# Kernel optimization log

Measured on AMD Instinct MI355X. Metric: run time of the kernel, lower is better.

## Reference

```python
import jax, jax.numpy as jnp
import numpy as np

DEG = 16

def setup_inputs() -> dict:
    key = jax.random.key(0)
    k1, k2 = jax.random.split(key)
    x = jax.random.uniform(k1, (2097152,), dtype=jnp.float32)  # in [0,1) subset of acos domain
    a = jax.random.normal(k2, (32, DEG), dtype=jnp.float32)
    return {"x": x, "a": a}

def reference(x, a):
    # Chebyshev basis T_k(x) = cos(k * acos(x)), shape [N, deg]
    k = jnp.arange(DEG, dtype=x.dtype)
    basis = jnp.cos(k[None, :] * jnp.arccos(x.reshape(-1))[:, None])  # [N, deg]
    coeffs = a.reshape(-1, DEG)  # [M, deg]
    # out[m, n] = sum_d coeffs[m, d] * basis[n, d]  -- a GEMM, not a 3D broadcast
    return jnp.einsum('md,nd->mn', coeffs, basis)
```

## Files before the change

kernel.cpp:

```cpp
#include <hip/hip_runtime.h>


#define DEG 16
#define M_ROWS 32
#define ELEMS_PER_THREAD 4

typedef __attribute__((ext_vector_type(2))) float f32x2;

__global__ __launch_bounds__(512) void dup_coeff_kernel(
    const float* __restrict__ a, f32x2* __restrict__ ad)
{
    const int i = threadIdx.x;
    if (i < M_ROWS * DEG) {
        const float c = a[i];
        f32x2 v; v.x = c; v.y = c;
        ad[i] = v;
    }
}

__global__ __launch_bounds__(256) void cheb_gemm_kernel(
    const float* __restrict__ x,
    const f32x2* __restrict__ ad,
    float* __restrict__ out,
    int n)
{
    const int i = (blockIdx.x * 256 + threadIdx.x) * ELEMS_PER_THREAD;
    if (i + ELEMS_PER_THREAD - 1 >= n) return;

    const float4 xv = *reinterpret_cast<const float4*>(x + i);

    f32x2 bA[DEG], bB[DEG];
    {
        f32x2 xA; xA.x = xv.x; xA.y = xv.y;
        f32x2 xB; xB.x = xv.z; xB.y = xv.w;
        f32x2 one; one.x = 1.0f; one.y = 1.0f;
        bA[0] = one; bB[0] = one;
        bA[1] = xA;  bB[1] = xB;
        const f32x2 txA = xA + xA;
        const f32x2 txB = xB + xB;
#pragma unroll
        for (int k = 2; k < DEG; ++k) {
            bA[k] = txA * bA[k - 1] - bA[k - 2];
            bB[k] = txB * bB[k - 1] - bB[k - 2];
        }
    }

#pragma unroll 4
    for (int m = 0; m < M_ROWS; ++m) {
        const f32x2* cm = ad + m * DEG;
        f32x2 accA, accB;
        {
            const f32x2 c0 = cm[0];
            asm("v_pk_mul_f32 %0, %1, %2" : "=v"(accA) : "s"(c0), "v"(bA[0]));
            asm("v_pk_mul_f32 %0, %1, %2" : "=v"(accB) : "s"(c0), "v"(bB[0]));
        }
#pragma unroll
        for (int d = 1; d < DEG; ++d) {
            const f32x2 cd = cm[d];
            asm("v_pk_fma_f32 %0, %1, %2, %0" : "+v"(accA) : "s"(cd), "v"(bA[d]));
            asm("v_pk_fma_f32 %0, %1, %2, %0" : "+v"(accB) : "s"(cd), "v"(bB[d]));
        }
        float4* dst = reinterpret_cast<float4*>(out + (size_t)m * (size_t)n + i);
        *dst = make_float4(accA.x, accA.y, accB.x, accB.y);
    }
}

extern "C" void kernel_launch(void* const* d_in, const int* in_sizes, int n_in,
                              void* d_out, int out_size, void* d_ws, size_t ws_size,
                              hipStream_t stream) {
    const float* x = (const float*)d_in[0];
    const float* a = (const float*)d_in[1];
    float* out = (float*)d_out;
    const int n = in_sizes[0];

    f32x2* ad = (f32x2*)d_ws;
    dup_coeff_kernel<<<1, 512, 0, stream>>>(a, ad);

    const int threads = 256;
    const int elems_per_block = threads * ELEMS_PER_THREAD;
    const int blocks = (n + elems_per_block - 1) / elems_per_block;

    cheb_gemm_kernel<<<blocks, threads, 0, stream>>>(x, ad, out, n);
}
```

Baseline: 56.19 us.

## Drop coefficient duplication kernel via op_sel broadcast and remap blocks per XCD

Removes the separate kernel that duplicated coefficients into f32x2 pairs. The main kernel now reads adjacent coefficient pairs directly and uses op_sel/op_sel_hi on the packed FMAs to broadcast either half of the scalar pair. This saves a launch and a dependent workspace write. It also remaps block indices so consecutive chunks land on the same XCD, which is meant to improve locality of x reads and output writes. The remap assumes gridDim is divisible by 8, which holds for this size.

```diff
diff --git a/kernel.cpp b/kernel.cpp
--- a/kernel.cpp
+++ b/kernel.cpp
@@ -4,27 +4,20 @@
 #define DEG 16
 #define M_ROWS 32
 #define ELEMS_PER_THREAD 4
+#define NUM_XCD 8
 
 typedef __attribute__((ext_vector_type(2))) float f32x2;
 
-__global__ __launch_bounds__(512) void dup_coeff_kernel(
-    const float* __restrict__ a, f32x2* __restrict__ ad)
-{
-    const int i = threadIdx.x;
-    if (i < M_ROWS * DEG) {
-        const float c = a[i];
-        f32x2 v; v.x = c; v.y = c;
-        ad[i] = v;
-    }
-}
-
 __global__ __launch_bounds__(256) void cheb_gemm_kernel(
     const float* __restrict__ x,
-    const f32x2* __restrict__ ad,
+    const float* __restrict__ a,
     float* __restrict__ out,
     int n)
 {
-    const int i = (blockIdx.x * 256 + threadIdx.x) * ELEMS_PER_THREAD;
+    const int per_xcd = gridDim.x >> 3;
+    const int chunk = (blockIdx.x & (NUM_XCD - 1)) * per_xcd
+                    + (blockIdx.x >> 3);
+    const int i = (chunk * 256 + threadIdx.x) * ELEMS_PER_THREAD;
     if (i + ELEMS_PER_THREAD - 1 >= n) return;
 
     const float4 xv = *reinterpret_cast<const float4*>(x + i);
@@ -47,18 +40,30 @@
 
 #pragma unroll 4
     for (int m = 0; m < M_ROWS; ++m) {
-        const f32x2* cm = ad + m * DEG;
+        const float* am = a + m * DEG;
         f32x2 accA, accB;
         {
-            const f32x2 c0 = cm[0];
-            asm("v_pk_mul_f32 %0, %1, %2" : "=v"(accA) : "s"(c0), "v"(bA[0]));
-            asm("v_pk_mul_f32 %0, %1, %2" : "=v"(accB) : "s"(c0), "v"(bB[0]));
+            const f32x2 c01 = *reinterpret_cast<const f32x2*>(am);
+            asm("v_pk_mul_f32 %0, %1, %2 op_sel:[0,0] op_sel_hi:[0,1]"
+                : "=v"(accA) : "s"(c01), "v"(bA[0]));
+            asm("v_pk_mul_f32 %0, %1, %2 op_sel:[0,0] op_sel_hi:[0,1]"
+                : "=v"(accB) : "s"(c01), "v"(bB[0]));
+            asm("v_pk_fma_f32 %0, %1, %2, %0 op_sel:[1,0,0] op_sel_hi:[1,1,1]"
+                : "+v"(accA) : "s"(c01), "v"(bA[1]));
+            asm("v_pk_fma_f32 %0, %1, %2, %0 op_sel:[1,0,0] op_sel_hi:[1,1,1]"
+                : "+v"(accB) : "s"(c01), "v"(bB[1]));
         }
 #pragma unroll
-        for (int d = 1; d < DEG; ++d) {
-            const f32x2 cd = cm[d];
-            asm("v_pk_fma_f32 %0, %1, %2, %0" : "+v"(accA) : "s"(cd), "v"(bA[d]));
-            asm("v_pk_fma_f32 %0, %1, %2, %0" : "+v"(accB) : "s"(cd), "v"(bB[d]));
+        for (int k = 1; k < DEG / 2; ++k) {
+            const f32x2 cp = *reinterpret_cast<const f32x2*>(am + 2 * k);
+            asm("v_pk_fma_f32 %0, %1, %2, %0 op_sel:[0,0,0] op_sel_hi:[0,1,1]"
+                : "+v"(accA) : "s"(cp), "v"(bA[2 * k]));
+            asm("v_pk_fma_f32 %0, %1, %2, %0 op_sel:[0,0,0] op_sel_hi:[0,1,1]"
+                : "+v"(accB) : "s"(cp), "v"(bB[2 * k]));
+            asm("v_pk_fma_f32 %0, %1, %2, %0 op_sel:[1,0,0] op_sel_hi:[1,1,1]"
+                : "+v"(accA) : "s"(cp), "v"(bA[2 * k + 1]));
+            asm("v_pk_fma_f32 %0, %1, %2, %0 op_sel:[1,0,0] op_sel_hi:[1,1,1]"
+                : "+v"(accB) : "s"(cp), "v"(bB[2 * k + 1]));
         }
         float4* dst = reinterpret_cast<float4*>(out + (size_t)m * (size_t)n + i);
         *dst = make_float4(accA.x, accA.y, accB.x, accB.y);
@@ -73,12 +78,9 @@
     float* out = (float*)d_out;
     const int n = in_sizes[0];
 
-    f32x2* ad = (f32x2*)d_ws;
-    dup_coeff_kernel<<<1, 512, 0, stream>>>(a, ad);
-
     const int threads = 256;
     const int elems_per_block = threads * ELEMS_PER_THREAD;
     const int blocks = (n + elems_per_block - 1) / elems_per_block;
 
-    cheb_gemm_kernel<<<blocks, threads, 0, stream>>>(x, ad, out, n);
+    cheb_gemm_kernel<<<blocks, threads, 0, stream>>>(x, a, out, n);
 }
```

New measurement: 48.63 us. 13.5% less time.
